# Kernel optimization log

Hardware: AMD Instinct MI355X
Metric: run time of the kernel (lower is better)

Reference implementation:

```python
import jax, jax.numpy as jnp
import numpy as np

LEAKY_SLOPE = 0.2  # tf.nn.leaky_relu default alpha
NEG_INF = -1e9


def setup_inputs() -> dict:
    key = jax.random.key(0)
    k1, k2, k3, k4 = jax.random.split(key, 4)
    B, N, F, D, H = 1, 4096, 128, 64, 4
    features = jax.random.normal(k1, (B, N, F), dtype=jnp.float32)
    adj = jax.random.randint(k2, (N, N), 0, 2, dtype=jnp.int32)  # 0/1 adjacency
    W = jax.random.normal(k3, (H, F, D), dtype=jnp.float32) * 0.1
    attn_k = jax.random.normal(k4, (H, 2 * D, 1), dtype=jnp.float32) * 0.1
    return {"adj": adj, "features": features, "W": W, "attn_k": attn_k}


def reference(adj, features, W, attn_k):
    H, _, D = W.shape
    adj_f = adj.astype(jnp.float32)[None]       # [1, N, N], broadcast over batch
    mask = adj_f != 0.0
    outs = []
    for i in range(H):  # fixed small head loop (heads are structurally distinct weights)
        h = features @ W[i]                      # [B, N, D]
        a_self = h @ attn_k[i, :D]               # [B, N, 1]
        a_neigh = h @ attn_k[i, D:]              # [B, N, 1]
        scores = a_self + jnp.swapaxes(a_neigh, 1, 2)  # [B, N, N] additive scores
        scores = jax.nn.leaky_relu(scores, LEAKY_SLOPE)
        scores = jnp.where(mask, scores, NEG_INF)
        attn = jax.nn.softmax(scores, axis=-1)   # [B, N, N]
        outs.append((attn * adj_f) @ h)          # [B, N, D]
    out = jnp.concatenate(outs, axis=-1) if H > 1 else outs[0]
    return jax.nn.relu(out)
```

## Files before the change

### kernel.cpp

```cpp
#include <hip/hip_runtime.h>
#include <math.h>

#define NN 4096
#define FF 128
#define DD 64
#define HH 4
#define NC 256

typedef _Float16 f16x8 __attribute__((ext_vector_type(8)));
typedef _Float16 f16x2 __attribute__((ext_vector_type(2)));
typedef float    f32x4 __attribute__((ext_vector_type(4)));

__global__ __launch_bounds__(256) void adjbits_kernel(
    const int* __restrict__ adj, unsigned int* __restrict__ adjw)
{
    const int w = blockIdx.x * 256 + threadIdx.x;
    const int4* __restrict__ p = (const int4*)(adj + (size_t)w * 32);
    unsigned int m = 0;
    #pragma unroll
    for (int i = 0; i < 8; ++i) {
        const int4 v = p[i];
        m |= (v.x != 0 ? 1u : 0u) << (i * 4);
        m |= (v.y != 0 ? 2u : 0u) << (i * 4);
        m |= (v.z != 0 ? 4u : 0u) << (i * 4);
        m |= (v.w != 0 ? 8u : 0u) << (i * 4);
    }
    adjw[w] = m;
}

__global__ __launch_bounds__(256) void prep_kernel(
    const float* __restrict__ feats, const float* __restrict__ W,
    const float* __restrict__ ak, _Float16* __restrict__ Bpack,
    _Float16* __restrict__ Es, _Float16* __restrict__ Fs,
    _Float16* __restrict__ En, _Float16* __restrict__ Fn)
{
    __shared__ float Wt[64 * 132];
    __shared__ float ft[32 * 128];
    __shared__ float hlds[32 * 65];
    const int t  = threadIdx.x;
    const int h  = blockIdx.y;
    const int n0 = blockIdx.x * 32;

    {
        const float* Wh = W + h * (FF * DD);
        #pragma unroll
        for (int j = 0; j < 8; ++j) {
            int idx = j * 256 + t;
            int f   = idx >> 4;
            int d4  = idx & 15;
            float4 v = ((const float4*)Wh)[idx];
            Wt[(d4 * 4 + 0) * 132 + f] = v.x;
            Wt[(d4 * 4 + 1) * 132 + f] = v.y;
            Wt[(d4 * 4 + 2) * 132 + f] = v.z;
            Wt[(d4 * 4 + 3) * 132 + f] = v.w;
        }
        #pragma unroll
        for (int j = 0; j < 4; ++j) {
            int idx = j * 256 + t;
            int r = idx >> 5, f4 = idx & 31;
            ((float4*)ft)[r * 32 + f4] = ((const float4*)feats)[(size_t)(n0 + r) * 32 + f4];
        }
    }
    __syncthreads();

    const int d   = t & 63;
    const int wid = t >> 6;
    float acc[8];
    #pragma unroll
    for (int j = 0; j < 8; ++j) acc[j] = 0.f;

    for (int f4 = 0; f4 < 32; ++f4) {
        const float4 w4 = *(const float4*)&Wt[d * 132 + f4 * 4];
        #pragma unroll
        for (int j = 0; j < 8; ++j) {
            const int r = wid + 4 * j;
            const float4 fv = *(const float4*)&ft[r * 128 + f4 * 4];
            acc[j] += fv.x * w4.x + fv.y * w4.y + fv.z * w4.z + fv.w * w4.w;
        }
    }

    const float aks = ak[h * 128 + d];
    const float akn = ak[h * 128 + 64 + d];
    #pragma unroll
    for (int j = 0; j < 8; ++j) {
        const int r = wid + 4 * j;
        const float hv = acc[j];
        hlds[r * 65 + d] = hv;
        float v1 = hv * aks;
        float v2 = hv * akn;
        #pragma unroll
        for (int m = 32; m >= 1; m >>= 1) {
            v1 += __shfl_xor(v1, m, 64);
            v2 += __shfl_xor(v2, m, 64);
        }
        if (d == 0) {
            Es[h * NN + n0 + r] = (_Float16)__expf(v1);
            Fs[h * NN + n0 + r] = (_Float16)__expf(0.2f * v1);
            En[h * NN + n0 + r] = (_Float16)__expf(v2);
            Fn[h * NN + n0 + r] = (_Float16)__expf(0.2f * v2);
        }
    }
    __syncthreads();

    const int cb = t >> 6;
    const int l  = t & 63;
    const int lr = l & 15;
    const int kg = l >> 4;
    f16x8 v;
    #pragma unroll
    for (int j = 0; j < 8; ++j)
        v[j] = (_Float16)hlds[(kg * 8 + j) * 65 + cb * 16 + lr];
    *(f16x8*)(Bpack + ((size_t)(h * 128 + blockIdx.x)) * 2048 + (cb * 64 + l) * 8) = v;
}

__global__ __launch_bounds__(256, 4) void attn_kernel(
    const unsigned int* __restrict__ adjw, const _Float16* __restrict__ Bpack,
    const _Float16* __restrict__ Es, const _Float16* __restrict__ Fs,
    const _Float16* __restrict__ En, const _Float16* __restrict__ Fn,
    float* __restrict__ pacc, float* __restrict__ pden, int ksplit)
{
    __shared__ _Float16 Blds[2][2048];

    const int t  = threadIdx.x;
    const int w  = t >> 6;
    const int l  = t & 63;
    const int lr = l & 15;
    const int kg = l >> 4;
    const int h  = blockIdx.y;
    const int s  = blockIdx.z;
    const int n0 = blockIdx.x * 128 + w * 32;

    const int mstart = s * ksplit;
    const int nchunk = ksplit >> 5;
    const int ncq    = nchunk >> 2;
    const int coff   = blockIdx.x & (ncq - 1);
    const int wb     = mstart >> 5;

#define PC(c) (((((c) >> 2) + coff) & (ncq - 1)) * 4 + ((c) & 3))

    const _Float16 es0 = Es[h * NN + n0 + lr],      fs0 = Fs[h * NN + n0 + lr];
    const _Float16 es1 = Es[h * NN + n0 + 16 + lr], fs1 = Fs[h * NN + n0 + 16 + lr];
    const f16x2 es20 = {es0, es0}, fs20 = {fs0, fs0};
    const f16x2 es21 = {es1, es1}, fs21 = {fs1, fs1};

    const _Float16* __restrict__ EnB = En + (size_t)h * NN;
    const _Float16* __restrict__ FnB = Fn + (size_t)h * NN;
    const int row0 = n0 + lr, row1 = n0 + 16 + lr;

    const _Float16* __restrict__ bp =
        Bpack + ((size_t)(h * 128) + wb) * 2048 + t * 8;

    f32x4 acc[2][4] = {};
    f32x4 dacc[2]   = {};
    f16x8 ones;
    #pragma unroll
    for (int j = 0; j < 8; ++j) ones[j] = (_Float16)1.0f;

    union U8 { f16x8 v; unsigned int u[4]; };

    uint4 sreg = *(const uint4*)(bp + (size_t)PC(0) * 2048);
    *(uint4*)&Blds[0][t * 8] = sreg;
    sreg = *(const uint4*)(bp + (size_t)PC(1) * 2048);
    uint4 enqc = *(const uint4*)(EnB + mstart + PC(0) * 32 + kg * 8);
    uint4 fnqc = *(const uint4*)(FnB + mstart + PC(0) * 32 + kg * 8);
    __syncthreads();

    for (int cq = 0; cq < ncq; ++cq) {
        const int cqp = (cq + coff) & (ncq - 1);
        const uint4 mk0 = *(const uint4*)&adjw[(size_t)row0 * 128 + wb + cqp * 4];
        const uint4 mk1 = *(const uint4*)&adjw[(size_t)row1 * 128 + wb + cqp * 4];

        #pragma unroll
        for (int ci = 0; ci < 4; ++ci) {
            const int c = cq * 4 + ci;

            uint4 nreg;
            {
                const int cn = (c + 2 < nchunk) ? c + 2 : c;
                nreg = *(const uint4*)(bp + (size_t)PC(cn) * 2048);
            }
            if (c + 1 < nchunk)
                *(uint4*)&Blds[(c + 1) & 1][t * 8] = sreg;
            uint4 enq_n, fnq_n;
            {
                const int cn = (c + 1 < nchunk) ? c + 1 : c;
                enq_n = *(const uint4*)(EnB + mstart + PC(cn) * 32 + kg * 8);
                fnq_n = *(const uint4*)(FnB + mstart + PC(cn) * 32 + kg * 8);
            }

            const unsigned int b0 =
                (ci == 0 ? mk0.x : ci == 1 ? mk0.y : ci == 2 ? mk0.z : mk0.w) >> (kg * 8);
            const unsigned int b1 =
                (ci == 0 ? mk1.x : ci == 1 ? mk1.y : ci == 2 ? mk1.z : mk1.w) >> (kg * 8);
            U8 A0, A1;
            #pragma unroll
            for (int p = 0; p < 4; ++p) {
                const unsigned int eu = p == 0 ? enqc.x : p == 1 ? enqc.y : p == 2 ? enqc.z : enqc.w;
                const unsigned int fu = p == 0 ? fnqc.x : p == 1 ? fnqc.y : p == 2 ? fnqc.z : fnqc.w;
                const f16x2 en2 = __builtin_bit_cast(f16x2, eu);
                const f16x2 fn2 = __builtin_bit_cast(f16x2, fu);
                const f16x2 v0 = __builtin_elementwise_max(es20 * en2, fs20 * fn2);
                const f16x2 v1 = __builtin_elementwise_max(es21 * en2, fs21 * fn2);
                const unsigned int mm0 = (((b0 >> (2 * p)) & 1u) ? 0x0000FFFFu : 0u)
                                       | (((b0 >> (2 * p + 1)) & 1u) ? 0xFFFF0000u : 0u);
                const unsigned int mm1 = (((b1 >> (2 * p)) & 1u) ? 0x0000FFFFu : 0u)
                                       | (((b1 >> (2 * p + 1)) & 1u) ? 0xFFFF0000u : 0u);
                A0.u[p] = __builtin_bit_cast(unsigned int, v0) & mm0;
                A1.u[p] = __builtin_bit_cast(unsigned int, v1) & mm1;
            }

            __builtin_amdgcn_s_setprio(1);
            #pragma unroll
            for (int cb = 0; cb < 4; ++cb) {
                const f16x8 Bf = *(const f16x8*)&Blds[c & 1][(cb * 64 + l) * 8];
                acc[0][cb] = __builtin_amdgcn_mfma_f32_16x16x32_f16(A0.v, Bf, acc[0][cb], 0, 0, 0);
                acc[1][cb] = __builtin_amdgcn_mfma_f32_16x16x32_f16(A1.v, Bf, acc[1][cb], 0, 0, 0);
            }
            dacc[0] = __builtin_amdgcn_mfma_f32_16x16x32_f16(A0.v, ones, dacc[0], 0, 0, 0);
            dacc[1] = __builtin_amdgcn_mfma_f32_16x16x32_f16(A1.v, ones, dacc[1], 0, 0, 0);
            __builtin_amdgcn_s_setprio(0);

            __syncthreads();
            sreg = nreg;
            enqc = enq_n;
            fnqc = fnq_n;
        }
    }
#undef PC

    #pragma unroll
    for (int rb = 0; rb < 2; ++rb) {
        #pragma unroll
        for (int r = 0; r < 4; ++r) {
            const int row = n0 + rb * 16 + kg * 4 + r;
            #pragma unroll
            for (int cb = 0; cb < 4; ++cb)
                pacc[((size_t)(s * NN + row)) * NC + h * 64 + cb * 16 + lr] = acc[rb][cb][r];
            if (lr == 0)
                pden[(s * NN + row) * 4 + h] = dacc[rb][r];
        }
    }
}

__global__ __launch_bounds__(256) void finalize_kernel(
    const float* __restrict__ pacc, const float* __restrict__ pden,
    float* __restrict__ out, int nsplit)
{
    const int t = threadIdx.x;
    const int n = blockIdx.x * 4 + (t >> 6);
    const int q = t & 63;
    const int h = q >> 4;

    f32x4 a = {0.f, 0.f, 0.f, 0.f};
    float d = 0.f;
    for (int s = 0; s < nsplit; ++s) {
        a += *(const f32x4*)&pacc[((size_t)(s * NN + n)) * NC + q * 4];
        d += pden[(s * NN + n) * 4 + h];
    }
    f32x4 o;
    const float inv = (d > 0.f) ? 1.0f / d : 0.f;
    #pragma unroll
    for (int i = 0; i < 4; ++i) {
        const float v = a[i] * inv;
        o[i] = v > 0.f ? v : 0.f;
    }
    *(f32x4*)&out[(size_t)n * NC + q * 4] = o;
}

extern "C" void kernel_launch(void* const* d_in, const int* in_sizes, int n_in,
                              void* d_out, int out_size, void* d_ws, size_t ws_size,
                              hipStream_t stream)
{
    const int*   adj   = (const int*)d_in[0];
    const float* feats = (const float*)d_in[1];
    const float* W     = (const float*)d_in[2];
    const float* ak    = (const float*)d_in[3];
    float*       out   = (float*)d_out;

    char* ws = (char*)d_ws;
    unsigned int* adjw  = (unsigned int*)ws;
    _Float16*     Bpack = (_Float16*)(ws + (2ull << 20));
    _Float16*     Es    = (_Float16*)(ws + (4ull << 20));
    _Float16*     Fs    = (_Float16*)(ws + (4ull << 20) + (1 << 16));
    _Float16*     En    = (_Float16*)(ws + (4ull << 20) + (2 << 16));
    _Float16*     Fn    = (_Float16*)(ws + (4ull << 20) + (3 << 16));
    float*        pden  = (float*)(ws + (4ull << 20) + (4 << 16));
    float*        pacc  = (float*)(ws + (5ull << 20));

    int nsplit = 8;
    while (nsplit > 1 && ws_size < (5ull << 20) + (size_t)nsplit * (4ull << 20))
        nsplit >>= 1;
    const int ksplit = NN / nsplit;

    adjbits_kernel<<<2048, 256, 0, stream>>>(adj, adjw);
    prep_kernel<<<dim3(128, 4), 256, 0, stream>>>(feats, W, ak, Bpack, Es, Fs, En, Fn);
    attn_kernel<<<dim3(32, 4, nsplit), 256, 0, stream>>>(adjw, Bpack, Es, Fs, En, Fn,
                                                         pacc, pden, ksplit);
    finalize_kernel<<<1024, 256, 0, stream>>>(pacc, pden, out, nsplit);
}
```

Baseline: 55.81 us.

## Coalesce adjacency bit-packing via LDS and use fp16 dot2 in projection

The adjacency packing kernel now reads int4s so that consecutive threads load consecutive addresses, stages per-element flag bytes in padded shared memory, and then assembles 32-bit masks per thread. This replaces the old strided per-thread reads. The feature projection in prep_kernel converts W and features to fp16 in shared memory and accumulates with fdot2 into fp32, which halves LDS traffic and packs two multiply-adds per instruction. The cost is reduced precision in h, which feeds the scores and the output.

```diff
diff --git a/kernel.cpp b/kernel.cpp
--- a/kernel.cpp
+++ b/kernel.cpp
@@ -8,24 +8,37 @@
 #define NC 256
 
 typedef _Float16 f16x8 __attribute__((ext_vector_type(8)));
+typedef _Float16 f16x4 __attribute__((ext_vector_type(4)));
 typedef _Float16 f16x2 __attribute__((ext_vector_type(2)));
 typedef float    f32x4 __attribute__((ext_vector_type(4)));
 
 __global__ __launch_bounds__(256) void adjbits_kernel(
     const int* __restrict__ adj, unsigned int* __restrict__ adjw)
 {
-    const int w = blockIdx.x * 256 + threadIdx.x;
-    const int4* __restrict__ p = (const int4*)(adj + (size_t)w * 32);
-    unsigned int m = 0;
+    __shared__ unsigned int fl[2304];
+    const int t = threadIdx.x;
+    const size_t e0 = (size_t)blockIdx.x * 8192;
+
     #pragma unroll
     for (int i = 0; i < 8; ++i) {
-        const int4 v = p[i];
-        m |= (v.x != 0 ? 1u : 0u) << (i * 4);
-        m |= (v.y != 0 ? 2u : 0u) << (i * 4);
-        m |= (v.z != 0 ? 4u : 0u) << (i * 4);
-        m |= (v.w != 0 ? 8u : 0u) << (i * 4);
-    }
-    adjw[w] = m;
+        const int4 v = ((const int4*)adj)[e0 / 4 + i * 256 + t];
+        const unsigned int b = (v.x != 0 ? 0x1u : 0u) |
+                               (v.y != 0 ? 0x100u : 0u) |
+                               (v.z != 0 ? 0x10000u : 0u) |
+                               (v.w != 0 ? 0x1000000u : 0u);
+        const int s = i * 256 + t;
+        fl[s + (s >> 3)] = b;
+    }
+    __syncthreads();
+
+    unsigned int w = 0;
+    #pragma unroll
+    for (int k = 0; k < 8; ++k) {
+        const unsigned int g = fl[t * 9 + k];
+        const unsigned int nib = (g | (g >> 7) | (g >> 14) | (g >> 21)) & 0xFu;
+        w |= nib << (k * 4);
+    }
+    adjw[blockIdx.x * 256 + t] = w;
 }
 
 __global__ __launch_bounds__(256) void prep_kernel(
@@ -34,9 +47,9 @@
     _Float16* __restrict__ Es, _Float16* __restrict__ Fs,
     _Float16* __restrict__ En, _Float16* __restrict__ Fn)
 {
-    __shared__ float Wt[64 * 132];
-    __shared__ float ft[32 * 128];
-    __shared__ float hlds[32 * 65];
+    __shared__ _Float16 Wth[64 * 136];
+    __shared__ _Float16 fth[32 * 128];
+    __shared__ float    hlds[32 * 65];
     const int t  = threadIdx.x;
     const int h  = blockIdx.y;
     const int n0 = blockIdx.x * 32;
@@ -49,16 +62,18 @@
             int f   = idx >> 4;
             int d4  = idx & 15;
             float4 v = ((const float4*)Wh)[idx];
-            Wt[(d4 * 4 + 0) * 132 + f] = v.x;
-            Wt[(d4 * 4 + 1) * 132 + f] = v.y;
-            Wt[(d4 * 4 + 2) * 132 + f] = v.z;
-            Wt[(d4 * 4 + 3) * 132 + f] = v.w;
+            Wth[(d4 * 4 + 0) * 136 + f] = (_Float16)v.x;
+            Wth[(d4 * 4 + 1) * 136 + f] = (_Float16)v.y;
+            Wth[(d4 * 4 + 2) * 136 + f] = (_Float16)v.z;
+            Wth[(d4 * 4 + 3) * 136 + f] = (_Float16)v.w;
         }
         #pragma unroll
         for (int j = 0; j < 4; ++j) {
             int idx = j * 256 + t;
             int r = idx >> 5, f4 = idx & 31;
-            ((float4*)ft)[r * 32 + f4] = ((const float4*)feats)[(size_t)(n0 + r) * 32 + f4];
+            float4 v = ((const float4*)feats)[(size_t)(n0 + r) * 32 + f4];
+            f16x4 hv = {(_Float16)v.x, (_Float16)v.y, (_Float16)v.z, (_Float16)v.w};
+            *(f16x4*)&fth[r * 128 + f4 * 4] = hv;
         }
     }
     __syncthreads();
@@ -69,13 +84,18 @@
     #pragma unroll
     for (int j = 0; j < 8; ++j) acc[j] = 0.f;
 
-    for (int f4 = 0; f4 < 32; ++f4) {
-        const float4 w4 = *(const float4*)&Wt[d * 132 + f4 * 4];
+    union UW { f16x8 v; unsigned int u[4]; };
+    for (int f8 = 0; f8 < 16; ++f8) {
+        UW w8; w8.v = *(const f16x8*)&Wth[d * 136 + f8 * 8];
         #pragma unroll
         for (int j = 0; j < 8; ++j) {
             const int r = wid + 4 * j;
-            const float4 fv = *(const float4*)&ft[r * 128 + f4 * 4];
-            acc[j] += fv.x * w4.x + fv.y * w4.y + fv.z * w4.z + fv.w * w4.w;
+            UW fv; fv.v = *(const f16x8*)&fth[r * 128 + f8 * 8];
+            #pragma unroll
+            for (int p = 0; p < 4; ++p)
+                acc[j] = __builtin_amdgcn_fdot2(
+                    __builtin_bit_cast(f16x2, w8.u[p]),
+                    __builtin_bit_cast(f16x2, fv.u[p]), acc[j], false);
         }
     }
 
```

Measured after the change: 59.81 us. 1.07x slower.
